# Performance work log

Measured on AMD Instinct MI355X. Metric: run time of the kernel, lower is better.

Reference implementation:

```python
import jax, jax.numpy as jnp
import numpy as np

B, S, D, E, TOP_K = 4, 4096, 2048, 64, 2


def setup_inputs() -> dict:
    key = jax.random.key(0)
    kx, kw, kb = jax.random.split(key, 3)
    x = jax.random.normal(kx, (B, S, D), dtype=jnp.float32)
    # nn.Linear(d_model, n_expert): weight (E, D), bias (E,)
    bound = 1.0 / np.sqrt(D)
    W = jax.random.uniform(kw, (E, D), dtype=jnp.float32, minval=-bound, maxval=bound)
    b = jax.random.uniform(kb, (E,), dtype=jnp.float32, minval=-bound, maxval=bound)
    return {"x": x, "W": W, "b": b}


def reference(x, W, b):
    # logits: (B, S, E)
    logits = jnp.einsum("bsd,ed->bse", x, W) + b
    top_k_logits, ids = jax.lax.top_k(logits, TOP_K)  # (B,S,K) each
    # scatter top-k logits into a -inf filled tensor along the expert dim
    n = B * S
    flat = jnp.full((n, E), -jnp.inf, dtype=logits.dtype)
    rows = jnp.arange(n)[:, None]  # (n,1)
    flat = flat.at[rows, ids.reshape(n, TOP_K)].set(top_k_logits.reshape(n, TOP_K))
    sparse_logits = flat.reshape(B, S, E)
    router_output = jax.nn.softmax(sparse_logits, axis=-1)  # zeros outside top-k
    return router_output, ids
```

## Files before the change

### kernel.cpp

```cpp
#include <hip/hip_runtime.h>
#include <math.h>

#define NTOK 16384
#define D_   2048
#define E_   64
#define TPB  16
#define NKC  (D_/32)

typedef _Float16 f16x8 __attribute__((ext_vector_type(8)));
typedef float    f32x4 __attribute__((ext_vector_type(4)));

#define LSCALE      256.0f
#define LSCALE2_INV (1.0f/65536.0f)

__global__ __launch_bounds__(256)
void prep_w(const float* __restrict__ W,
            _Float16* __restrict__ wh, _Float16* __restrict__ wl)
{
    const int idx = blockIdx.x * 256 + threadIdx.x;
    const int l  = idx & 63;
    const int kc = (idx >> 6) & 63;
    const int nt = idx >> 12;
    const int e  = nt * 16 + (l & 15);
    const int g  = l >> 4;
    const float* src = W + (size_t)e * D_ + kc * 32 + g * 4;
    const float4 f0 = *reinterpret_cast<const float4*>(src);
    const float4 f1 = *reinterpret_cast<const float4*>(src + 16);
    const float v[8] = {f0.x, f0.y, f0.z, f0.w, f1.x, f1.y, f1.z, f1.w};
    f16x8 h, lo;
#pragma unroll
    for (int j = 0; j < 8; ++j) {
        const float vs = v[j] * LSCALE;
        const _Float16 hj = (_Float16)vs;
        h[j]  = hj;
        lo[j] = (_Float16)(vs - (float)hj);
    }
    *reinterpret_cast<f16x8*>(wh + (size_t)idx * 8) = h;
    *reinterpret_cast<f16x8*>(wl + (size_t)idx * 8) = lo;
}

__global__ __launch_bounds__(64, 1)
void router_mfma(const float* __restrict__ x,
                 const _Float16* __restrict__ wh,
                 const _Float16* __restrict__ wl,
                 const float* __restrict__ bias,
                 float* __restrict__ out)
{
    __shared__ float smem[TPB * 65 + TPB * 4];

    const int l  = threadIdx.x;
    const int T0 = blockIdx.x * TPB;
    const int g  = l >> 4;

    const float* xp = x + (size_t)(T0 + (l & 15)) * D_ + g * 4;
    const _Float16* bh_b = wh + (size_t)l * 8;
    const _Float16* bl_b = wl + (size_t)l * 8;

    f32x4 acc0 = {0.f,0.f,0.f,0.f}, acc1 = {0.f,0.f,0.f,0.f};
    f32x4 acc2 = {0.f,0.f,0.f,0.f}, acc3 = {0.f,0.f,0.f,0.f};

    float4 xa[4], xb[4];
    f16x8  BH[4][4], BL[4][4];

#pragma unroll
    for (int j = 0; j < 4; ++j) {
        xa[j] = *reinterpret_cast<const float4*>(xp + j * 32);
        xb[j] = *reinterpret_cast<const float4*>(xp + j * 32 + 16);
#pragma unroll
        for (int nt = 0; nt < 4; ++nt) {
            BH[j][nt] = *reinterpret_cast<const f16x8*>(bh_b + nt * 32768 + j * 512);
            BL[j][nt] = *reinterpret_cast<const f16x8*>(bl_b + nt * 32768 + j * 512);
        }
    }

    for (int s = 0; s < 15; ++s) {
        const int K = s << 2;
#pragma unroll
        for (int j = 0; j < 4; ++j) {
            f16x8 ah, al_;
            {
                float vs;
                vs = xa[j].x * LSCALE; ah[0] = (_Float16)vs; al_[0] = (_Float16)(vs - (float)ah[0]);
                vs = xa[j].y * LSCALE; ah[1] = (_Float16)vs; al_[1] = (_Float16)(vs - (float)ah[1]);
                vs = xa[j].z * LSCALE; ah[2] = (_Float16)vs; al_[2] = (_Float16)(vs - (float)ah[2]);
                vs = xa[j].w * LSCALE; ah[3] = (_Float16)vs; al_[3] = (_Float16)(vs - (float)ah[3]);
                vs = xb[j].x * LSCALE; ah[4] = (_Float16)vs; al_[4] = (_Float16)(vs - (float)ah[4]);
                vs = xb[j].y * LSCALE; ah[5] = (_Float16)vs; al_[5] = (_Float16)(vs - (float)ah[5]);
                vs = xb[j].z * LSCALE; ah[6] = (_Float16)vs; al_[6] = (_Float16)(vs - (float)ah[6]);
                vs = xb[j].w * LSCALE; ah[7] = (_Float16)vs; al_[7] = (_Float16)(vs - (float)ah[7]);
            }
            acc0 = __builtin_amdgcn_mfma_f32_16x16x32_f16(ah,  BH[j][0], acc0, 0, 0, 0);
            acc0 = __builtin_amdgcn_mfma_f32_16x16x32_f16(al_, BH[j][0], acc0, 0, 0, 0);
            acc0 = __builtin_amdgcn_mfma_f32_16x16x32_f16(ah,  BL[j][0], acc0, 0, 0, 0);
            acc1 = __builtin_amdgcn_mfma_f32_16x16x32_f16(ah,  BH[j][1], acc1, 0, 0, 0);
            acc1 = __builtin_amdgcn_mfma_f32_16x16x32_f16(al_, BH[j][1], acc1, 0, 0, 0);
            acc1 = __builtin_amdgcn_mfma_f32_16x16x32_f16(ah,  BL[j][1], acc1, 0, 0, 0);
            acc2 = __builtin_amdgcn_mfma_f32_16x16x32_f16(ah,  BH[j][2], acc2, 0, 0, 0);
            acc2 = __builtin_amdgcn_mfma_f32_16x16x32_f16(al_, BH[j][2], acc2, 0, 0, 0);
            acc2 = __builtin_amdgcn_mfma_f32_16x16x32_f16(ah,  BL[j][2], acc2, 0, 0, 0);
            acc3 = __builtin_amdgcn_mfma_f32_16x16x32_f16(ah,  BH[j][3], acc3, 0, 0, 0);
            acc3 = __builtin_amdgcn_mfma_f32_16x16x32_f16(al_, BH[j][3], acc3, 0, 0, 0);
            acc3 = __builtin_amdgcn_mfma_f32_16x16x32_f16(ah,  BL[j][3], acc3, 0, 0, 0);
            {
                const int kn = K + j + 4;
                xa[j] = *reinterpret_cast<const float4*>(xp + kn * 32);
                xb[j] = *reinterpret_cast<const float4*>(xp + kn * 32 + 16);
#pragma unroll
                for (int nt = 0; nt < 4; ++nt) {
                    BH[j][nt] = *reinterpret_cast<const f16x8*>(bh_b + nt * 32768 + (size_t)kn * 512);
                    BL[j][nt] = *reinterpret_cast<const f16x8*>(bl_b + nt * 32768 + (size_t)kn * 512);
                }
            }
            __builtin_amdgcn_sched_barrier(0);
        }
    }
#pragma unroll
    for (int j = 0; j < 4; ++j) {
        f16x8 ah, al_;
        {
            float vs;
            vs = xa[j].x * LSCALE; ah[0] = (_Float16)vs; al_[0] = (_Float16)(vs - (float)ah[0]);
            vs = xa[j].y * LSCALE; ah[1] = (_Float16)vs; al_[1] = (_Float16)(vs - (float)ah[1]);
            vs = xa[j].z * LSCALE; ah[2] = (_Float16)vs; al_[2] = (_Float16)(vs - (float)ah[2]);
            vs = xa[j].w * LSCALE; ah[3] = (_Float16)vs; al_[3] = (_Float16)(vs - (float)ah[3]);
            vs = xb[j].x * LSCALE; ah[4] = (_Float16)vs; al_[4] = (_Float16)(vs - (float)ah[4]);
            vs = xb[j].y * LSCALE; ah[5] = (_Float16)vs; al_[5] = (_Float16)(vs - (float)ah[5]);
            vs = xb[j].z * LSCALE; ah[6] = (_Float16)vs; al_[6] = (_Float16)(vs - (float)ah[6]);
            vs = xb[j].w * LSCALE; ah[7] = (_Float16)vs; al_[7] = (_Float16)(vs - (float)ah[7]);
        }
        acc0 = __builtin_amdgcn_mfma_f32_16x16x32_f16(ah,  BH[j][0], acc0, 0, 0, 0);
        acc0 = __builtin_amdgcn_mfma_f32_16x16x32_f16(al_, BH[j][0], acc0, 0, 0, 0);
        acc0 = __builtin_amdgcn_mfma_f32_16x16x32_f16(ah,  BL[j][0], acc0, 0, 0, 0);
        acc1 = __builtin_amdgcn_mfma_f32_16x16x32_f16(ah,  BH[j][1], acc1, 0, 0, 0);
        acc1 = __builtin_amdgcn_mfma_f32_16x16x32_f16(al_, BH[j][1], acc1, 0, 0, 0);
        acc1 = __builtin_amdgcn_mfma_f32_16x16x32_f16(ah,  BL[j][1], acc1, 0, 0, 0);
        acc2 = __builtin_amdgcn_mfma_f32_16x16x32_f16(ah,  BH[j][2], acc2, 0, 0, 0);
        acc2 = __builtin_amdgcn_mfma_f32_16x16x32_f16(al_, BH[j][2], acc2, 0, 0, 0);
        acc2 = __builtin_amdgcn_mfma_f32_16x16x32_f16(ah,  BL[j][2], acc2, 0, 0, 0);
        acc3 = __builtin_amdgcn_mfma_f32_16x16x32_f16(ah,  BH[j][3], acc3, 0, 0, 0);
        acc3 = __builtin_amdgcn_mfma_f32_16x16x32_f16(al_, BH[j][3], acc3, 0, 0, 0);
        acc3 = __builtin_amdgcn_mfma_f32_16x16x32_f16(ah,  BL[j][3], acc3, 0, 0, 0);
    }

    {
        const int col = l & 15;
#pragma unroll
        for (int r = 0; r < 4; ++r) {
            const int t = g * 4 + r;
            smem[t * 65 + 0  + col] = acc0[r] * LSCALE2_INV;
            smem[t * 65 + 16 + col] = acc1[r] * LSCALE2_INV;
            smem[t * 65 + 32 + col] = acc2[r] * LSCALE2_INV;
            smem[t * 65 + 48 + col] = acc3[r] * LSCALE2_INV;
        }
    }
    __syncthreads();

    float* res = smem + TPB * 65;
    if (l < TPB) {
        const float* lg = smem + l * 65;
        float m1 = -INFINITY, m2 = -INFINITY;
        int i1 = 0, i2 = 0;
        for (int e = 0; e < E_; ++e) {
            const float v = lg[e] + bias[e];
            if (v > m1)      { m2 = m1; i2 = i1; m1 = v; i1 = e; }
            else if (v > m2) { m2 = v;  i2 = e; }
        }
        const float ex  = expf(m2 - m1);
        const float den = 1.f + ex;
        res[l*4+0] = 1.f / den;
        res[l*4+1] = ex / den;
        res[l*4+2] = (float)i1;
        res[l*4+3] = (float)i2;
    }
    __syncthreads();

    float* ob = out + (size_t)T0 * E_;
#pragma unroll
    for (int i = 0; i < 4; ++i) {
        const int idx = i * 256 + l * 4;
        const int t   = idx >> 6;
        const int e0  = idx & 63;
        const float p1 = res[t*4+0];
        const float p2 = res[t*4+1];
        const int   i1 = (int)res[t*4+2];
        const int   i2 = (int)res[t*4+3];
        float4 v;
        v.x = (e0+0 == i1) ? p1 : ((e0+0 == i2) ? p2 : 0.f);
        v.y = (e0+1 == i1) ? p1 : ((e0+1 == i2) ? p2 : 0.f);
        v.z = (e0+2 == i1) ? p1 : ((e0+2 == i2) ? p2 : 0.f);
        v.w = (e0+3 == i1) ? p1 : ((e0+3 == i2) ? p2 : 0.f);
        *reinterpret_cast<float4*>(ob + idx) = v;
    }
    if (l < TPB * 2) {
        out[(size_t)NTOK * E_ + (size_t)T0 * 2 + l] =
            res[(l >> 1) * 4 + 2 + (l & 1)];
    }
}

extern "C" void kernel_launch(void* const* d_in, const int* in_sizes, int n_in,
                              void* d_out, int out_size, void* d_ws, size_t ws_size,
                              hipStream_t stream) {
    const float* x = (const float*)d_in[0];
    const float* W = (const float*)d_in[1];
    const float* b = (const float*)d_in[2];
    float* out     = (float*)d_out;
    _Float16* wh   = (_Float16*)d_ws;
    _Float16* wl   = wh + (size_t)4 * NKC * 64 * 8;

    hipLaunchKernelGGL(prep_w, dim3(64), dim3(256), 0, stream, W, wh, wl);
    hipLaunchKernelGGL(router_mfma, dim3(NTOK / TPB), dim3(64), 0, stream,
                       x, wh, wl, b, out);
}
```

Baseline: 49.52 us.

## Run eight waves per block, each covering eight tokens of a 64-token tile

The block grows from one wave handling 16 tokens to eight waves covering 64 tokens. Each wave loads only 8 distinct token rows (lanes 8-15 duplicate lanes 0-7), so half of each wave's MFMA output rows are thrown away. The intent is more waves per CU to hide latency, and the block's waves may share the weight loads in cache. The trade-off is doubled MFMA work per token, up to 512-way register pressure under the launch bounds, and fewer blocks (256) across the GPU.

```diff
diff --git a/kernel.cpp b/kernel.cpp
--- a/kernel.cpp
+++ b/kernel.cpp
@@ -4,7 +4,7 @@
 #define NTOK 16384
 #define D_   2048
 #define E_   64
-#define TPB  16
+#define TPB  64
 #define NKC  (D_/32)
 
 typedef _Float16 f16x8 __attribute__((ext_vector_type(8)));
@@ -39,7 +39,7 @@
     *reinterpret_cast<f16x8*>(wl + (size_t)idx * 8) = lo;
 }
 
-__global__ __launch_bounds__(64, 1)
+__global__ __launch_bounds__(512, 2)
 void router_mfma(const float* __restrict__ x,
                  const _Float16* __restrict__ wh,
                  const _Float16* __restrict__ wl,
@@ -48,11 +48,13 @@
 {
     __shared__ float smem[TPB * 65 + TPB * 4];
 
-    const int l  = threadIdx.x;
-    const int T0 = blockIdx.x * TPB;
-    const int g  = l >> 4;
-
-    const float* xp = x + (size_t)(T0 + (l & 15)) * D_ + g * 4;
+    const int tid = threadIdx.x;
+    const int l   = tid & 63;
+    const int w   = __builtin_amdgcn_readfirstlane(tid >> 6);
+    const int T0  = blockIdx.x * TPB;
+    const int g   = l >> 4;
+
+    const float* xp = x + (size_t)(T0 + w * 8 + (l & 7)) * D_ + g * 4;
     const _Float16* bh_b = wh + (size_t)l * 8;
     const _Float16* bl_b = wl + (size_t)l * 8;
 
@@ -142,11 +144,11 @@
         acc3 = __builtin_amdgcn_mfma_f32_16x16x32_f16(ah,  BL[j][3], acc3, 0, 0, 0);
     }
 
-    {
+    if (g < 2) {
         const int col = l & 15;
 #pragma unroll
         for (int r = 0; r < 4; ++r) {
-            const int t = g * 4 + r;
+            const int t = w * 8 + g * 4 + r;
             smem[t * 65 + 0  + col] = acc0[r] * LSCALE2_INV;
             smem[t * 65 + 16 + col] = acc1[r] * LSCALE2_INV;
             smem[t * 65 + 32 + col] = acc2[r] * LSCALE2_INV;
@@ -156,8 +158,8 @@
     __syncthreads();
 
     float* res = smem + TPB * 65;
-    if (l < TPB) {
-        const float* lg = smem + l * 65;
+    if (tid < TPB) {
+        const float* lg = smem + tid * 65;
         float m1 = -INFINITY, m2 = -INFINITY;
         int i1 = 0, i2 = 0;
         for (int e = 0; e < E_; ++e) {
@@ -167,17 +169,17 @@
         }
         const float ex  = expf(m2 - m1);
         const float den = 1.f + ex;
-        res[l*4+0] = 1.f / den;
-        res[l*4+1] = ex / den;
-        res[l*4+2] = (float)i1;
-        res[l*4+3] = (float)i2;
+        res[tid*4+0] = 1.f / den;
+        res[tid*4+1] = ex / den;
+        res[tid*4+2] = (float)i1;
+        res[tid*4+3] = (float)i2;
     }
     __syncthreads();
 
     float* ob = out + (size_t)T0 * E_;
 #pragma unroll
-    for (int i = 0; i < 4; ++i) {
-        const int idx = i * 256 + l * 4;
+    for (int i = 0; i < 2; ++i) {
+        const int idx = i * 2048 + tid * 4;
         const int t   = idx >> 6;
         const int e0  = idx & 63;
         const float p1 = res[t*4+0];
@@ -191,9 +193,9 @@
         v.w = (e0+3 == i1) ? p1 : ((e0+3 == i2) ? p2 : 0.f);
         *reinterpret_cast<float4*>(ob + idx) = v;
     }
-    if (l < TPB * 2) {
-        out[(size_t)NTOK * E_ + (size_t)T0 * 2 + l] =
-            res[(l >> 1) * 4 + 2 + (l & 1)];
+    if (tid < TPB * 2) {
+        out[(size_t)NTOK * E_ + (size_t)T0 * 2 + tid] =
+            res[(tid >> 1) * 4 + 2 + (tid & 1)];
     }
 }
 
@@ -208,6 +210,6 @@
     _Float16* wl   = wh + (size_t)4 * NKC * 64 * 8;
 
     hipLaunchKernelGGL(prep_w, dim3(64), dim3(256), 0, stream, W, wh, wl);
-    hipLaunchKernelGGL(router_mfma, dim3(NTOK / TPB), dim3(64), 0, stream,
+    hipLaunchKernelGGL(router_mfma, dim3(NTOK / TPB), dim3(512), 0, stream,
                        x, wh, wl, b, out);
 }
```

Measured after the change: 75.87 us. 1.53x slower.
